# Kernel optimization log

Measured on AMD Instinct MI355X. Metric: run time of the kernel, lower is better.

Reference implementation:

```python
import jax, jax.numpy as jnp
import numpy as np

N_NODES = 50000
N_EDGES = 800000
D_IN, D_HID, D_OUT = 128, 128, 64


def setup_inputs() -> dict:
    key = jax.random.key(0)
    ks = jax.random.split(key, 8)
    x = jax.random.normal(ks[0], (N_NODES, D_IN), dtype=jnp.float32)
    edge_index = jax.random.randint(ks[1], (2, N_EDGES), 0, N_NODES, dtype=jnp.int64)
    s1 = 1.0 / np.sqrt(D_IN)
    s2 = 1.0 / np.sqrt(D_HID)
    return {
        "x": x,
        "edge_index": edge_index,
        "W1_l": jax.random.normal(ks[2], (D_IN, D_HID), dtype=jnp.float32) * s1,
        "W1_r": jax.random.normal(ks[3], (D_IN, D_HID), dtype=jnp.float32) * s1,
        "b1": jnp.zeros((D_HID,), dtype=jnp.float32),
        "W2_l": jax.random.normal(ks[4], (D_HID, D_OUT), dtype=jnp.float32) * s2,
        "W2_r": jax.random.normal(ks[5], (D_HID, D_OUT), dtype=jnp.float32) * s2,
        "b2": jnp.zeros((D_OUT,), dtype=jnp.float32),
    }


def _sage_conv(x, src, dst, W_l, W_r, b, num_nodes):
    # SAGEConv (PyG defaults): mean-aggregate neighbor features, then
    # out = mean_j x_j @ W_l + x_i @ W_r + b
    msg = x[src]                                                  # [E, D] gather
    agg = jax.ops.segment_sum(msg, dst, num_segments=num_nodes)   # [N, D] scatter-add
    ones = jnp.ones((src.shape[0],), dtype=x.dtype)
    deg = jax.ops.segment_sum(ones, dst, num_segments=num_nodes)  # [N]
    mean = agg / jnp.maximum(deg, 1.0)[:, None]
    return mean @ W_l + x @ W_r + b


def reference(x, edge_index, W1_l, W1_r, b1, W2_l, W2_r, b2):
    n = x.shape[0]
    src, dst = edge_index[0], edge_index[1]
    h = jax.nn.relu(_sage_conv(x, src, dst, W1_l, W1_r, b1, n))
    return _sage_conv(h, src, dst, W2_l, W2_r, b2, n)
```

## Files before the change

kernel.cpp:

```cpp
#include <hip/hip_runtime.h>

#define D_IN  128
#define D_HID 128
#define D_OUT 64
#define NPB   256
#define CH    4096
#define CBKT  5120

typedef __attribute__((ext_vector_type(8))) short bf16x8;
typedef __attribute__((ext_vector_type(4))) float f32x4;

__device__ __forceinline__ short f2bf(float f) {
    union { float f; unsigned u; } cv; cv.f = f;
    unsigned r = (cv.u + 0x7FFFu + ((cv.u >> 16) & 1u)) >> 16;
    return (short)r;
}
__device__ __forceinline__ float bf2f(short s) {
    union { unsigned u; float f; } cv;
    cv.u = ((unsigned)(unsigned short)s) << 16;
    return cv.f;
}

__global__ void conv_bf16_strided(const float* __restrict__ in, short* __restrict__ xcat,
                                  long nrows) {
    long t = (long)blockIdx.x * blockDim.x + threadIdx.x;
    if (t >= nrows * 16) return;
    long row = t >> 4;
    int c = ((int)t & 15) << 3;
    const float* p = in + row * 128 + c;
    float4 v0 = *(const float4*)p;
    float4 v1 = *(const float4*)(p + 4);
    short* o = xcat + row * 256 + 128 + c;
    short4 o0 = { f2bf(v0.x), f2bf(v0.y), f2bf(v0.z), f2bf(v0.w) };
    short4 o1 = { f2bf(v1.x), f2bf(v1.y), f2bf(v1.z), f2bf(v1.w) };
    *(short4*)o = o0;
    *(short4*)(o + 4) = o1;
}

__global__ void build_wt_all(const float* __restrict__ W1l, const float* __restrict__ W1r,
                             const float* __restrict__ W2l, const float* __restrict__ W2r,
                             short* __restrict__ wt1, short* __restrict__ wt2,
                             int* __restrict__ pcur) {
    if (blockIdx.x == 0) pcur[threadIdx.x] = 0;
    int idx = blockIdx.x * blockDim.x + threadIdx.x;
    if (idx < 128 * 256) {
        int c = idx >> 8, k = idx & 255;
        float v = (k < 128) ? W1l[k * 128 + c] : W1r[(k - 128) * 128 + c];
        wt1[idx] = f2bf(v);
    } else {
        int j = idx - 128 * 256;
        int c = j >> 7, k = j & 127;
        float v = (c < 64) ? W2l[k * 64 + c] : W2r[k * 64 + (c - 64)];
        wt2[j] = f2bf(v);
    }
}

__global__ void bucket_fill(const int* __restrict__ src, const int* __restrict__ dst,
                            int* __restrict__ pcur, int* __restrict__ pairs, int E) {
    __shared__ int lh[256];
    __shared__ int lbase[256];
    __shared__ int lcur[256];
    const int t = threadIdx.x;
    for (long cbase = (long)blockIdx.x * CH; cbase < E; cbase += (long)gridDim.x * CH) {
        int lo = (int)cbase;
        int hi = min(E, lo + CH);
        lh[t] = 0;
        __syncthreads();
        for (int e = lo + t; e < hi; e += 256)
            atomicAdd(&lh[dst[e] >> 8], 1);
        __syncthreads();
        int c = lh[t];
        lbase[t] = t * CBKT + (c ? atomicAdd(&pcur[t], c) : 0);
        lcur[t] = 0;
        __syncthreads();
        for (int e = lo + t; e < hi; e += 256) {
            int d = dst[e];
            int b = d >> 8;
            int off = atomicAdd(&lcur[b], 1);
            pairs[lbase[b] + off] = ((d & (NPB - 1)) << 16) | src[e];
        }
        __syncthreads();
    }
}

__global__ void node_fill(const int* __restrict__ pairs, const int* __restrict__ pcur,
                          int* __restrict__ cnt, int* __restrict__ beg,
                          int* __restrict__ col, int N) {
    __shared__ int h[256];
    __shared__ int s[256];
    const int t = threadIdx.x;
    const int b = blockIdx.x;
    const int lo = b << 8;
    const int p0 = b * CBKT;
    const int p1 = p0 + pcur[b];

    h[t] = 0;
    __syncthreads();
    for (int p = p0 + t; p < p1; p += 256)
        atomicAdd(&h[pairs[p] >> 16], 1);
    __syncthreads();
    int v = h[t];
    s[t] = v;
    __syncthreads();
    for (int off = 1; off < 256; off <<= 1) {
        int u = (t >= off) ? s[t - off] : 0;
        __syncthreads();
        s[t] += u;
        __syncthreads();
    }
    int excl = s[t] - v;
    __syncthreads();
    s[t] = p0 + excl;
    h[t] = 0;
    int i = lo + t;
    if (i < N) { cnt[i] = v; beg[i] = p0 + excl; }
    __syncthreads();
    for (int p = p0 + t; p < p1; p += 256) {
        int pr = pairs[p];
        int nl = pr >> 16;
        int off = atomicAdd(&h[nl], 1);
        col[s[nl] + off] = pr & 0xFFFF;
    }
}

__global__ void gather_mean1(short* __restrict__ xcat,
                             const int* __restrict__ beg, const int* __restrict__ cnt,
                             const int* __restrict__ col, int N) {
    constexpr int G = 16;
    long t = (long)blockIdx.x * blockDim.x + threadIdx.x;
    long i = t / G;
    if (i >= N) return;
    int c = ((int)(t % G)) << 3;

    int b0 = beg[i];
    int deg = cnt[i];
    int end = b0 + deg;
    float a[8] = {0.f, 0.f, 0.f, 0.f, 0.f, 0.f, 0.f, 0.f};
    int e = b0;
    for (; e + 3 < end; e += 4) {
        int s0 = col[e], s1 = col[e + 1], s2 = col[e + 2], s3 = col[e + 3];
        bf16x8 v0 = *(const bf16x8*)(xcat + (long)s0 * 256 + 128 + c);
        bf16x8 v1 = *(const bf16x8*)(xcat + (long)s1 * 256 + 128 + c);
        bf16x8 v2 = *(const bf16x8*)(xcat + (long)s2 * 256 + 128 + c);
        bf16x8 v3 = *(const bf16x8*)(xcat + (long)s3 * 256 + 128 + c);
        #pragma unroll
        for (int q = 0; q < 8; ++q)
            a[q] += (bf2f(v0[q]) + bf2f(v1[q])) + (bf2f(v2[q]) + bf2f(v3[q]));
    }
    for (; e < end; ++e) {
        bf16x8 v0 = *(const bf16x8*)(xcat + (long)col[e] * 256 + 128 + c);
        #pragma unroll
        for (int q = 0; q < 8; ++q) a[q] += bf2f(v0[q]);
    }
    float inv = 1.0f / fmaxf((float)deg, 1.0f);
    short4 lo4 = { f2bf(a[0] * inv), f2bf(a[1] * inv), f2bf(a[2] * inv), f2bf(a[3] * inv) };
    short4 hi4 = { f2bf(a[4] * inv), f2bf(a[5] * inv), f2bf(a[6] * inv), f2bf(a[7] * inv) };
    *(short4*)(xcat + i * 256 + c) = lo4;
    *(short4*)(xcat + i * 256 + c + 4) = hi4;
}

__global__ __launch_bounds__(256)
void gemm1_fused(const short* __restrict__ A, const short* __restrict__ Wt,
                 const float* __restrict__ bias, short* __restrict__ H,
                 int N, int nTiles) {
    const int wid  = threadIdx.x >> 6;
    const int lane = threadIdx.x & 63;
    const int colBase = wid * 32;
    const int l15 = lane & 15;
    const int kq  = lane >> 4;

    bf16x8 b[8][2];
    #pragma unroll
    for (int s = 0; s < 8; ++s)
        #pragma unroll
        for (int f = 0; f < 2; ++f)
            b[s][f] = *(const bf16x8*)(Wt + (long)(colBase + f * 16 + l15) * 256 + s * 32 + kq * 8);

    float bv[2];
    #pragma unroll
    for (int f = 0; f < 2; ++f) bv[f] = bias[colBase + f * 16 + l15];

    auto loadA = [&](bf16x8 (&a)[8], long tile) {
        long row = tile * 16 + l15;
        row = row < N ? row : (long)N - 1;
        const short* ap = A + row * 256 + kq * 8;
        #pragma unroll
        for (int s = 0; s < 8; ++s)
            a[s] = *(const bf16x8*)(ap + s * 32);
    };

    auto computeStore = [&](bf16x8 (&a)[8], long tile) {
        f32x4 acc[2] = {};
        #pragma unroll
        for (int s = 0; s < 8; ++s) {
            acc[0] = __builtin_amdgcn_mfma_f32_16x16x32_bf16(a[s], b[s][0], acc[0], 0, 0, 0);
            acc[1] = __builtin_amdgcn_mfma_f32_16x16x32_bf16(a[s], b[s][1], acc[1], 0, 0, 0);
        }
        long rb = tile * 16;
        #pragma unroll
        for (int f = 0; f < 2; ++f) {
            int colv = colBase + f * 16 + l15;
            #pragma unroll
            for (int j = 0; j < 4; ++j) {
                long row = rb + kq * 4 + j;
                if (row < N)
                    H[row * 128 + colv] = f2bf(fmaxf(acc[f][j] + bv[f], 0.f));
            }
        }
    };

    long t = blockIdx.x;
    const long stride = gridDim.x;
    bf16x8 a0[8], a1[8];
    if (t < nTiles) loadA(a0, t);
    bool cur0 = true;
    for (; t < nTiles; t += stride) {
        long tn = t + stride;
        if (cur0) {
            if (tn < nTiles) loadA(a1, tn);
            __builtin_amdgcn_sched_barrier(0);
            computeStore(a0, t);
        } else {
            if (tn < nTiles) loadA(a0, tn);
            __builtin_amdgcn_sched_barrier(0);
            computeStore(a1, t);
        }
        cur0 = !cur0;
    }
}

template<int NCOLS, int LEFT, int FR>
__global__ __launch_bounds__(256)
void gemm_dual_pipe(const short* __restrict__ A, const short* __restrict__ Wt,
                    const float* __restrict__ bias,
                    short* __restrict__ outL, short* __restrict__ outR,
                    int N, int nTiles) {
    constexpr int K = 128;
    constexpr int WC = NCOLS / 64;
    constexpr int WR = 4 / WC;
    constexpr int BM = WR * FR * 16;
    constexpr int RIGHT = NCOLS - LEFT;

    const int wid  = threadIdx.x >> 6;
    const int lane = threadIdx.x & 63;
    const int wc = wid % WC, wr = wid / WC;
    const int colBase = wc * 64;
    const int l15 = lane & 15;
    const int kq  = lane >> 4;
    const int rowOff = wr * (FR * 16);

    bf16x8 b[4][4];
    #pragma unroll
    for (int s = 0; s < 4; ++s)
        #pragma unroll
        for (int f = 0; f < 4; ++f)
            b[s][f] = *(const bf16x8*)(Wt + (long)(colBase + f * 16 + l15) * K + s * 32 + kq * 8);

    float bv[4];
    #pragma unroll
    for (int f = 0; f < 4; ++f) {
        int col = colBase + f * 16 + l15;
        bv[f] = (col >= LEFT) ? bias[col - LEFT] : 0.f;
    }

    auto loadA = [&](bf16x8 (&a)[4][FR], long tile) {
        long rb = tile * BM + rowOff;
        #pragma unroll
        for (int s = 0; s < 4; ++s) {
            int ko = s * 32 + kq * 8;
            #pragma unroll
            for (int r = 0; r < FR; ++r) {
                long row = rb + r * 16 + l15;
                row = row < N ? row : (long)N - 1;
                a[s][r] = *(const bf16x8*)(A + row * K + ko);
            }
        }
    };

    auto computeStore = [&](bf16x8 (&a)[4][FR], long tile) {
        f32x4 acc[FR][4] = {};
        #pragma unroll
        for (int s = 0; s < 4; ++s)
            #pragma unroll
            for (int r = 0; r < FR; ++r)
                #pragma unroll
                for (int f = 0; f < 4; ++f)
                    acc[r][f] = __builtin_amdgcn_mfma_f32_16x16x32_bf16(a[s][r], b[s][f], acc[r][f], 0, 0, 0);
        long rb = tile * BM + rowOff;
        #pragma unroll
        for (int r = 0; r < FR; ++r) {
            #pragma unroll
            for (int f = 0; f < 4; ++f) {
                int col = colBase + f * 16 + l15;
                #pragma unroll
                for (int j = 0; j < 4; ++j) {
                    long row = rb + r * 16 + kq * 4 + j;
                    if (row < N) {
                        float v = acc[r][f][j];
                        if (col < LEFT) outL[row * LEFT + col] = f2bf(v);
                        else            outR[row * RIGHT + (col - LEFT)] = f2bf(v + bv[f]);
                    }
                }
            }
        }
    };

    long t = blockIdx.x;
    const long stride = gridDim.x;
    bf16x8 a0[4][FR], a1[4][FR];
    if (t < nTiles) loadA(a0, t);
    bool cur0 = true;
    for (; t < nTiles; t += stride) {
        long tn = t + stride;
        if (cur0) {
            if (tn < nTiles) loadA(a1, tn);
            __builtin_amdgcn_sched_barrier(0);
            computeStore(a0, t);
        } else {
            if (tn < nTiles) loadA(a0, tn);
            __builtin_amdgcn_sched_barrier(0);
            computeStore(a1, t);
        }
        cur0 = !cur0;
    }
}

__global__ void gather_final(const short* __restrict__ gl, const short* __restrict__ rr,
                             const int* __restrict__ beg, const int* __restrict__ cnt,
                             const int* __restrict__ col, float* __restrict__ outp, int N) {
    constexpr int M = 64;
    constexpr int G = 8;
    long t = (long)blockIdx.x * blockDim.x + threadIdx.x;
    long i = t / G;
    if (i >= N) return;
    int c = ((int)(t % G)) << 3;

    int b0 = beg[i];
    int deg = cnt[i];
    int end = b0 + deg;
    float a[8] = {0.f, 0.f, 0.f, 0.f, 0.f, 0.f, 0.f, 0.f};
    int e = b0;
    for (; e + 3 < end; e += 4) {
        int s0 = col[e], s1 = col[e + 1], s2 = col[e + 2], s3 = col[e + 3];
        bf16x8 v0 = *(const bf16x8*)(gl + (long)s0 * M + c);
        bf16x8 v1 = *(const bf16x8*)(gl + (long)s1 * M + c);
        bf16x8 v2 = *(const bf16x8*)(gl + (long)s2 * M + c);
        bf16x8 v3 = *(const bf16x8*)(gl + (long)s3 * M + c);
        #pragma unroll
        for (int q = 0; q < 8; ++q)
            a[q] += (bf2f(v0[q]) + bf2f(v1[q])) + (bf2f(v2[q]) + bf2f(v3[q]));
    }
    for (; e < end; ++e) {
        bf16x8 v0 = *(const bf16x8*)(gl + (long)col[e] * M + c);
        #pragma unroll
        for (int q = 0; q < 8; ++q) a[q] += bf2f(v0[q]);
    }

    float inv = 1.0f / fmaxf((float)deg, 1.0f);
    bf16x8 rv = *(const bf16x8*)(rr + i * M + c);
    float4 lo4 = { fmaf(a[0], inv, bf2f(rv[0])), fmaf(a[1], inv, bf2f(rv[1])),
                   fmaf(a[2], inv, bf2f(rv[2])), fmaf(a[3], inv, bf2f(rv[3])) };
    float4 hi4 = { fmaf(a[4], inv, bf2f(rv[4])), fmaf(a[5], inv, bf2f(rv[5])),
                   fmaf(a[6], inv, bf2f(rv[6])), fmaf(a[7], inv, bf2f(rv[7])) };
    *(float4*)(outp + i * M + c) = lo4;
    *(float4*)(outp + i * M + c + 4) = hi4;
}

extern "C" void kernel_launch(void* const* d_in, const int* in_sizes, int n_in,
                              void* d_out, int out_size, void* d_ws, size_t ws_size,
                              hipStream_t stream) {
    const float* x   = (const float*)d_in[0];
    const int*   ei  = (const int*)  d_in[1];
    const float* W1l = (const float*)d_in[2];
    const float* W1r = (const float*)d_in[3];
    const float* b1  = (const float*)d_in[4];
    const float* W2l = (const float*)d_in[5];
    const float* W2r = (const float*)d_in[6];
    const float* b2  = (const float*)d_in[7];
    float* out = (float*)d_out;

    const int N = in_sizes[0] / D_IN;
    const int E = in_sizes[1] / 2;
    const int* src = ei;
    const int* dst = ei + E;
    const int NB = (N + NPB - 1) / NPB;

    short* xcat = (short*)d_ws;
    short* hb   = xcat + (size_t)N * 256;
    short* hlb  = hb + (size_t)N * 128;
    short* hrb  = hlb + (size_t)N * 64;
    short* wt1  = hrb + (size_t)N * 64;
    short* wt2  = wt1 + 128 * 256;
    int* pcur   = (int*)(wt2 + 128 * 128);
    int* cnt    = pcur + 256;
    int* beg    = cnt + N;
    int* pairs  = beg + N;
    int* colArr = pairs + (size_t)NB * CBKT;

    conv_bf16_strided<<<(int)(((long)N * 16 + 255) / 256), 256, 0, stream>>>(x, xcat, N);
    build_wt_all<<<(128 * 256 + 128 * 128) / 256, 256, 0, stream>>>(W1l, W1r, W2l, W2r,
                                                                    wt1, wt2, pcur);
    bucket_fill<<<(E + CH - 1) / CH, 256, 0, stream>>>(src, dst, pcur, pairs, E);
    node_fill<<<NB, 256, 0, stream>>>(pairs, pcur, cnt, beg, colArr, N);

    gather_mean1<<<(int)(((long)N * 16 + 255) / 256), 256, 0, stream>>>(xcat, beg, cnt, colArr, N);
    {
        int nT = (N + 15) / 16;
        gemm1_fused<<<1024, 256, 0, stream>>>(xcat, wt1, b1, hb, N, nT);
    }

    {
        int nT = (N + 63) / 64;
        gemm_dual_pipe<128, 64, 2><<<384, 256, 0, stream>>>(hb, wt2, b2, hlb, hrb, N, nT);
    }
    gather_final<<<(int)(((long)N * 8 + 255) / 256), 256, 0, stream>>>(hlb, hrb, beg, cnt,
                                                                       colArr, out, N);
}
```

Measured before the change: 126.2 us.

## Fuse layer-1 neighbor mean gather into GEMM via shared-memory tile

Merges the bf16 conversion, weight packing and counter reset into one prep kernel. It also replaces the separate layer-1 gather kernel and persistent GEMM with one fused kernel. That kernel gathers and averages neighbor rows for 16 nodes into shared memory next to each node's own features, then runs the MFMA GEMM from LDS. This drops the write and re-read of the aggregated half of the concatenated buffer and two launches. In exchange it loses the persistent double-buffered GEMM loop and reloads the weight fragments in every 16-row block.

```diff
diff --git a/kernel.cpp b/kernel.cpp
--- a/kernel.cpp
+++ b/kernel.cpp
@@ -21,37 +21,36 @@
     return cv.f;
 }
 
-__global__ void conv_bf16_strided(const float* __restrict__ in, short* __restrict__ xcat,
-                                  long nrows) {
+__global__ void prep(const float* __restrict__ x, short* __restrict__ xb,
+                     const float* __restrict__ W1l, const float* __restrict__ W1r,
+                     const float* __restrict__ W2l, const float* __restrict__ W2r,
+                     short* __restrict__ wt1, short* __restrict__ wt2,
+                     int* __restrict__ pcur, int N) {
     long t = (long)blockIdx.x * blockDim.x + threadIdx.x;
-    if (t >= nrows * 16) return;
-    long row = t >> 4;
-    int c = ((int)t & 15) << 3;
-    const float* p = in + row * 128 + c;
-    float4 v0 = *(const float4*)p;
-    float4 v1 = *(const float4*)(p + 4);
-    short* o = xcat + row * 256 + 128 + c;
-    short4 o0 = { f2bf(v0.x), f2bf(v0.y), f2bf(v0.z), f2bf(v0.w) };
-    short4 o1 = { f2bf(v1.x), f2bf(v1.y), f2bf(v1.z), f2bf(v1.w) };
-    *(short4*)o = o0;
-    *(short4*)(o + 4) = o1;
-}
-
-__global__ void build_wt_all(const float* __restrict__ W1l, const float* __restrict__ W1r,
-                             const float* __restrict__ W2l, const float* __restrict__ W2r,
-                             short* __restrict__ wt1, short* __restrict__ wt2,
-                             int* __restrict__ pcur) {
-    if (blockIdx.x == 0) pcur[threadIdx.x] = 0;
-    int idx = blockIdx.x * blockDim.x + threadIdx.x;
-    if (idx < 128 * 256) {
+    long nconv = (long)N * 16;
+    if (t < nconv) {
+        long row = t >> 4;
+        int c = ((int)t & 15) << 3;
+        const float* p = x + row * 128 + c;
+        float4 v0 = *(const float4*)p;
+        float4 v1 = *(const float4*)(p + 4);
+        short4 o0 = { f2bf(v0.x), f2bf(v0.y), f2bf(v0.z), f2bf(v0.w) };
+        short4 o1 = { f2bf(v1.x), f2bf(v1.y), f2bf(v1.z), f2bf(v1.w) };
+        short* o = xb + row * 128 + c;
+        *(short4*)o = o0;
+        *(short4*)(o + 4) = o1;
+    } else if (t < nconv + 128 * 256) {
+        int idx = (int)(t - nconv);
         int c = idx >> 8, k = idx & 255;
         float v = (k < 128) ? W1l[k * 128 + c] : W1r[(k - 128) * 128 + c];
         wt1[idx] = f2bf(v);
-    } else {
-        int j = idx - 128 * 256;
+    } else if (t < nconv + 128 * 256 + 128 * 128) {
+        int j = (int)(t - nconv - 128 * 256);
         int c = j >> 7, k = j & 127;
         float v = (c < 64) ? W2l[k * 64 + c] : W2r[k * 64 + (c - 64)];
         wt2[j] = f2bf(v);
+    } else if (t < nconv + 128 * 256 + 128 * 128 + 256) {
+        pcur[(int)(t - nconv - 128 * 256 - 128 * 128)] = 0;
     }
 }
 
@@ -123,51 +122,18 @@
     }
 }
 
-__global__ void gather_mean1(short* __restrict__ xcat,
-                             const int* __restrict__ beg, const int* __restrict__ cnt,
-                             const int* __restrict__ col, int N) {
-    constexpr int G = 16;
-    long t = (long)blockIdx.x * blockDim.x + threadIdx.x;
-    long i = t / G;
-    if (i >= N) return;
-    int c = ((int)(t % G)) << 3;
-
-    int b0 = beg[i];
-    int deg = cnt[i];
-    int end = b0 + deg;
-    float a[8] = {0.f, 0.f, 0.f, 0.f, 0.f, 0.f, 0.f, 0.f};
-    int e = b0;
-    for (; e + 3 < end; e += 4) {
-        int s0 = col[e], s1 = col[e + 1], s2 = col[e + 2], s3 = col[e + 3];
-        bf16x8 v0 = *(const bf16x8*)(xcat + (long)s0 * 256 + 128 + c);
-        bf16x8 v1 = *(const bf16x8*)(xcat + (long)s1 * 256 + 128 + c);
-        bf16x8 v2 = *(const bf16x8*)(xcat + (long)s2 * 256 + 128 + c);
-        bf16x8 v3 = *(const bf16x8*)(xcat + (long)s3 * 256 + 128 + c);
-        #pragma unroll
-        for (int q = 0; q < 8; ++q)
-            a[q] += (bf2f(v0[q]) + bf2f(v1[q])) + (bf2f(v2[q]) + bf2f(v3[q]));
-    }
-    for (; e < end; ++e) {
-        bf16x8 v0 = *(const bf16x8*)(xcat + (long)col[e] * 256 + 128 + c);
-        #pragma unroll
-        for (int q = 0; q < 8; ++q) a[q] += bf2f(v0[q]);
-    }
-    float inv = 1.0f / fmaxf((float)deg, 1.0f);
-    short4 lo4 = { f2bf(a[0] * inv), f2bf(a[1] * inv), f2bf(a[2] * inv), f2bf(a[3] * inv) };
-    short4 hi4 = { f2bf(a[4] * inv), f2bf(a[5] * inv), f2bf(a[6] * inv), f2bf(a[7] * inv) };
-    *(short4*)(xcat + i * 256 + c) = lo4;
-    *(short4*)(xcat + i * 256 + c + 4) = hi4;
-}
-
 __global__ __launch_bounds__(256)
-void gemm1_fused(const short* __restrict__ A, const short* __restrict__ Wt,
-                 const float* __restrict__ bias, short* __restrict__ H,
-                 int N, int nTiles) {
-    const int wid  = threadIdx.x >> 6;
-    const int lane = threadIdx.x & 63;
+void fused_layer1(const short* __restrict__ xb, const short* __restrict__ Wt,
+                  const float* __restrict__ bias,
+                  const int* __restrict__ beg, const int* __restrict__ cnt,
+                  const int* __restrict__ col, short* __restrict__ H, int N) {
+    __shared__ short xs[16][264];
+    const int tid = threadIdx.x;
+    const long row0 = (long)blockIdx.x * 16;
+
+    const int wid = tid >> 6, lane = tid & 63;
     const int colBase = wid * 32;
-    const int l15 = lane & 15;
-    const int kq  = lane >> 4;
+    const int l15 = lane & 15, kq = lane >> 4;
 
     bf16x8 b[8][2];
     #pragma unroll
@@ -175,57 +141,62 @@
         #pragma unroll
         for (int f = 0; f < 2; ++f)
             b[s][f] = *(const bf16x8*)(Wt + (long)(colBase + f * 16 + l15) * 256 + s * 32 + kq * 8);
-
     float bv[2];
     #pragma unroll
     for (int f = 0; f < 2; ++f) bv[f] = bias[colBase + f * 16 + l15];
 
-    auto loadA = [&](bf16x8 (&a)[8], long tile) {
-        long row = tile * 16 + l15;
-        row = row < N ? row : (long)N - 1;
-        const short* ap = A + row * 256 + kq * 8;
-        #pragma unroll
-        for (int s = 0; s < 8; ++s)
-            a[s] = *(const bf16x8*)(ap + s * 32);
-    };
-
-    auto computeStore = [&](bf16x8 (&a)[8], long tile) {
-        f32x4 acc[2] = {};
-        #pragma unroll
-        for (int s = 0; s < 8; ++s) {
-            acc[0] = __builtin_amdgcn_mfma_f32_16x16x32_bf16(a[s], b[s][0], acc[0], 0, 0, 0);
-            acc[1] = __builtin_amdgcn_mfma_f32_16x16x32_bf16(a[s], b[s][1], acc[1], 0, 0, 0);
-        }
-        long rb = tile * 16;
-        #pragma unroll
-        for (int f = 0; f < 2; ++f) {
-            int colv = colBase + f * 16 + l15;
-            #pragma unroll
-            for (int j = 0; j < 4; ++j) {
-                long row = rb + kq * 4 + j;
-                if (row < N)
-                    H[row * 128 + colv] = f2bf(fmaxf(acc[f][j] + bv[f], 0.f));
-            }
-        }
-    };
-
-    long t = blockIdx.x;
-    const long stride = gridDim.x;
-    bf16x8 a0[8], a1[8];
-    if (t < nTiles) loadA(a0, t);
-    bool cur0 = true;
-    for (; t < nTiles; t += stride) {
-        long tn = t + stride;
-        if (cur0) {
-            if (tn < nTiles) loadA(a1, tn);
-            __builtin_amdgcn_sched_barrier(0);
-            computeStore(a0, t);
-        } else {
-            if (tn < nTiles) loadA(a0, tn);
-            __builtin_amdgcn_sched_barrier(0);
-            computeStore(a1, t);
-        }
-        cur0 = !cur0;
+    const int r  = tid >> 4;
+    const int c  = (tid & 15) << 3;
+    long row = row0 + r;
+    float a[8] = {0.f, 0.f, 0.f, 0.f, 0.f, 0.f, 0.f, 0.f};
+    int deg = 0;
+    if (row < N) {
+        int b0 = beg[row];
+        deg = cnt[row];
+        int end = b0 + deg;
+        int e = b0;
+        for (; e + 3 < end; e += 4) {
+            int s0 = col[e], s1 = col[e + 1], s2 = col[e + 2], s3 = col[e + 3];
+            bf16x8 v0 = *(const bf16x8*)(xb + (long)s0 * 128 + c);
+            bf16x8 v1 = *(const bf16x8*)(xb + (long)s1 * 128 + c);
+            bf16x8 v2 = *(const bf16x8*)(xb + (long)s2 * 128 + c);
+            bf16x8 v3 = *(const bf16x8*)(xb + (long)s3 * 128 + c);
+            #pragma unroll
+            for (int q = 0; q < 8; ++q)
+                a[q] += (bf2f(v0[q]) + bf2f(v1[q])) + (bf2f(v2[q]) + bf2f(v3[q]));
+        }
+        for (; e < end; ++e) {
+            bf16x8 v0 = *(const bf16x8*)(xb + (long)col[e] * 128 + c);
+            #pragma unroll
+            for (int q = 0; q < 8; ++q) a[q] += bf2f(v0[q]);
+        }
+    }
+    float inv = 1.0f / fmaxf((float)deg, 1.0f);
+    short4 m0 = { f2bf(a[0] * inv), f2bf(a[1] * inv), f2bf(a[2] * inv), f2bf(a[3] * inv) };
+    short4 m1 = { f2bf(a[4] * inv), f2bf(a[5] * inv), f2bf(a[6] * inv), f2bf(a[7] * inv) };
+    *(short4*)(&xs[r][c]) = m0;
+    *(short4*)(&xs[r][c + 4]) = m1;
+    long rowc = row < N ? row : (long)N - 1;
+    *(bf16x8*)(&xs[r][128 + c]) = *(const bf16x8*)(xb + rowc * 128 + c);
+    __syncthreads();
+
+    f32x4 acc[2] = {};
+    #pragma unroll
+    for (int s = 0; s < 8; ++s) {
+        bf16x8 af = *(const bf16x8*)(&xs[l15][s * 32 + kq * 8]);
+        acc[0] = __builtin_amdgcn_mfma_f32_16x16x32_bf16(af, b[s][0], acc[0], 0, 0, 0);
+        acc[1] = __builtin_amdgcn_mfma_f32_16x16x32_bf16(af, b[s][1], acc[1], 0, 0, 0);
+    }
+
+    #pragma unroll
+    for (int f = 0; f < 2; ++f) {
+        int colv = colBase + f * 16 + l15;
+        #pragma unroll
+        for (int j = 0; j < 4; ++j) {
+            long rw = row0 + kq * 4 + j;
+            if (rw < N)
+                H[rw * 128 + colv] = f2bf(fmaxf(acc[f][j] + bv[f], 0.f));
+        }
     }
 }
 
@@ -385,8 +356,8 @@
     const int* dst = ei + E;
     const int NB = (N + NPB - 1) / NPB;
 
-    short* xcat = (short*)d_ws;
-    short* hb   = xcat + (size_t)N * 256;
+    short* xb   = (short*)d_ws;
+    short* hb   = xb + (size_t)N * 128;
     short* hlb  = hb + (size_t)N * 128;
     short* hrb  = hlb + (size_t)N * 64;
     short* wt1  = hrb + (size_t)N * 64;
@@ -397,17 +368,15 @@
     int* pairs  = beg + N;
     int* colArr = pairs + (size_t)NB * CBKT;
 
-    conv_bf16_strided<<<(int)(((long)N * 16 + 255) / 256), 256, 0, stream>>>(x, xcat, N);
-    build_wt_all<<<(128 * 256 + 128 * 128) / 256, 256, 0, stream>>>(W1l, W1r, W2l, W2r,
-                                                                    wt1, wt2, pcur);
+    {
+        long tot = (long)N * 16 + 128 * 256 + 128 * 128 + 256;
+        prep<<<(int)((tot + 255) / 256), 256, 0, stream>>>(x, xb, W1l, W1r, W2l, W2r,
+                                                           wt1, wt2, pcur, N);
+    }
     bucket_fill<<<(E + CH - 1) / CH, 256, 0, stream>>>(src, dst, pcur, pairs, E);
     node_fill<<<NB, 256, 0, stream>>>(pairs, pcur, cnt, beg, colArr, N);
 
-    gather_mean1<<<(int)(((long)N * 16 + 255) / 256), 256, 0, stream>>>(xcat, beg, cnt, colArr, N);
-    {
-        int nT = (N + 15) / 16;
-        gemm1_fused<<<1024, 256, 0, stream>>>(xcat, wt1, b1, hb, N, nT);
-    }
+    fused_layer1<<<(N + 15) / 16, 256, 0, stream>>>(xb, wt1, b1, beg, cnt, colArr, hb, N);
 
     {
         int nT = (N + 63) / 64;
```

Measured after the change: 136.0 us. 7.8% more time.
